# Kernel tuning notes

Measured on AMD Instinct MI355X. Metric: run time of the kernel, lower is better.

## Reference

```python
import jax, jax.numpy as jnp
import numpy as np


def setup_inputs() -> dict:
    key = jax.random.key(0)
    k1, k2 = jax.random.split(key)
    B, S, H, D = 4, 2048, 12, 64
    v = jax.random.normal(k1, (B, S, H, D), dtype=jnp.float32)
    # learned per-head positional weights, sorted ascending along last dim
    # (mirrors torch.sort(torch.randn(H, S), dim=-1)[0])
    w = jnp.sort(jax.random.normal(k2, (H, S), dtype=jnp.float32), axis=-1)
    return {"v": v, "w": w}


def reference(v, w):
    # PositionalBias._naive
    # v: [B, S, H, D]; w: [H, S_max]
    B, S, H, D = v.shape
    seq_len = S - 2  # v[:, 1:-1] is the non-special-token span
    w_ = w[:, :seq_len]  # [H, seq_len]
    # _construct_bias builds bias[h, l, j] = w[h, |l - j|] (symmetric Toeplitz)
    pos = jnp.arange(seq_len)
    idx = jnp.abs(pos[:, None] - pos[None, :])  # [seq_len, seq_len]
    bias = w_[:, idx]  # [H, seq_len, seq_len]
    # zero-pad one row/col on each side -> [H, S, S]
    bias = jnp.pad(bias, ((0, 0), (1, 1), (1, 1)))
    # z_pb: [1, S, H]
    z_pb = jnp.sum(bias, axis=-1).T[None, :, :]
    # pbv: [B, S, H, D]
    pbv = jnp.einsum('nlhd,hlj->njhd', v, bias)
    return (pbv, z_pb)
```

## Files before the change

kernel.cpp:

```cpp
#include <hip/hip_runtime.h>
#include <hip/hip_bf16.h>


typedef short short8 __attribute__((ext_vector_type(8)));
typedef float floatx4 __attribute__((ext_vector_type(4)));

typedef const __attribute__((address_space(1))) void gvoid_t;
typedef __attribute__((address_space(3))) void lvoid_t;

__device__ __forceinline__ unsigned short f2bf(float f) {
  union { __hip_bfloat16 b; unsigned short u; } cv;
  cv.b = __float2bfloat16(f);
  return cv.u;
}

__global__ __launch_bounds__(256) void transpose_kernel(const float* __restrict__ v,
                                                        unsigned short* __restrict__ vb) {
  __shared__ float tile[64][65];
  const int lt = blockIdx.x;
  const int h  = blockIdx.y;
  const int n  = blockIdx.z;
  const int tid = threadIdx.x;
  const int l0 = lt * 64;
  {
    const int d  = tid & 63;
    const int r0 = tid >> 6;
    #pragma unroll
    for (int rr = 0; rr < 16; ++rr) {
      int ll = r0 * 16 + rr;
      tile[ll][d] = v[(((size_t)n * 2048 + (l0 + ll)) * 12 + h) * 64 + d];
    }
  }
  __syncthreads();
  {
    const int d = tid >> 2;
    const int q = tid & 3;
    unsigned short buf[16] __attribute__((aligned(16)));
    #pragma unroll
    for (int jj = 0; jj < 16; ++jj) {
      int l = l0 + q * 16 + jj;
      float f = tile[q * 16 + jj][d];
      buf[jj] = (l == 0 || l == 2047) ? (unsigned short)0 : f2bf(f);
    }
    unsigned short* dst = vb + ((size_t)h * 256 + n * 64 + d) * 2048 + l0 + q * 16;
    *(uint4*)dst       = *(const uint4*)&buf[0];
    *(uint4*)(dst + 8) = *(const uint4*)&buf[8];
  }
}

__global__ __launch_bounds__(256) void zpb_kernel(const float* __restrict__ w,
                                                  float* __restrict__ zout) {
  __shared__ float wv[2048];
  __shared__ float pfx[2048];
  __shared__ float wsum[4];
  const int h = blockIdx.x;
  const int tid = threadIdx.x;
  const float* wh = w + (size_t)h * 2048;
  for (int i = tid; i < 2048; i += 256) wv[i] = (i < 2046) ? wh[i] : 0.f;
  __syncthreads();
  const int base = tid * 8;
  float run0 = 0.f;
  #pragma unroll
  for (int k = 0; k < 8; ++k) run0 += wv[base + k];
  float x = run0;
  #pragma unroll
  for (int d = 1; d < 64; d <<= 1) {
    float y = __shfl_up(x, d);
    if ((tid & 63) >= d) x += y;
  }
  if ((tid & 63) == 63) wsum[tid >> 6] = x;
  __syncthreads();
  const int wid = tid >> 6;
  float woff = 0.f;
  #pragma unroll
  for (int u = 0; u < 3; ++u) { float t = wsum[u]; if (u < wid) woff += t; }
  float excl = x + woff - run0;
  float pr = excl;
  #pragma unroll
  for (int k = 0; k < 8; ++k) { pr += wv[base + k]; pfx[base + k] = pr; }
  __syncthreads();
  for (int i = tid; i < 2046; i += 256) {
    float z = pfx[i] + pfx[2045 - i] - wv[0];
    zout[(size_t)(i + 1) * 12 + h] = z;
  }
  if (tid == 0) { zout[h] = 0.f; zout[(size_t)2047 * 12 + h] = 0.f; }
}

__global__ __launch_bounds__(256, 2) void gemm_kernel(const float* __restrict__ w,
                                                      const unsigned short* __restrict__ vb,
                                                      float* __restrict__ out) {
  __shared__ __attribute__((aligned(16))) short Tls[8 * 2184];
  __shared__ __attribute__((aligned(16))) short vt[2][128][32];

  const int jt  = blockIdx.x;
  const int ndt = blockIdx.y;
  const int h   = blockIdx.z;
  const int tid = threadIdx.x;
  const int lane = tid & 63;
  const int wid  = tid >> 6;
  const int wm = wid >> 1, wn = wid & 1;
  const int lm = lane & 15, quad = lane >> 4;
  const int jb = jt * 128;

  const float* wh = w + (size_t)h * 2048;
  for (int g = tid; g < 8 * 273; g += 256) {
    int c  = g / 273;
    int p8 = (g - c * 273) * 8;
    unsigned short buf[8] __attribute__((aligned(16)));
    #pragma unroll
    for (int i = 0; i < 8; ++i) {
      int t = 127 + jb - (p8 + i) - c;
      int a = t < 0 ? -t : t;
      buf[i] = (a <= 2045) ? f2bf(wh[a]) : (unsigned short)0;
    }
    *(short8*)&Tls[c * 2184 + p8] = *(const short8*)buf;
  }
  __syncthreads();

  const int nd0 = ndt * 128;
  const int jw  = jb + wm * 64;
  const int ndw = nd0 + wn * 64;
  const unsigned short* vbp = vb + (size_t)h * 256 * 2048;

  floatx4 acc[4][4];
  #pragma unroll
  for (int ma = 0; ma < 4; ++ma)
    #pragma unroll
    for (int na = 0; na < 4; ++na)
      acc[ma][na] = (floatx4){0.f, 0.f, 0.f, 0.f};

  const int pbase = 127 + quad * 8 - wm * 64 - lm;
  auto load_af = [&](int g16, int l0) -> short8 {
    int p0 = l0 + g16 + pbase;
    int c  = p0 & 7;
    return *(const short8*)&Tls[c * 2184 + (p0 - c)];
  };

  short8 a4 = load_af(-48, 0);
  short8 a5 = load_af(-32, 0);

  #pragma unroll 1
  for (int l0 = 0; l0 < 2048; l0 += 64) {
    #pragma unroll
    for (int s = 0; s < 2; ++s) {
      #pragma unroll
      for (int u = 0; u < 2; ++u) {
        int e  = wid * 2 + u;
        int r0 = e * 16;
        int grow = nd0 + r0 + (lane >> 2);
        int gcol = l0 + s * 32 + (lane & 3) * 8;
        const unsigned short* g = vbp + (size_t)grow * 2048 + gcol;
        __builtin_amdgcn_global_load_lds((gvoid_t*)g, (lvoid_t*)&vt[s][r0][0], 16, 0, 0);
      }
    }
    asm volatile("s_waitcnt vmcnt(0)" ::: "memory");
    __syncthreads();

    short8 afr[6];
    afr[0] = a4; afr[1] = a5;
    afr[2] = load_af(-16, l0);
    afr[3] = load_af(0,   l0);
    afr[4] = load_af(16,  l0);
    afr[5] = load_af(32,  l0);
    a4 = afr[4]; a5 = afr[5];

    #pragma unroll
    for (int kc = 0; kc < 2; ++kc) {
      short8 bfr[4];
      #pragma unroll
      for (int na = 0; na < 4; ++na)
        bfr[na] = *(const short8*)&vt[kc][wn * 64 + na * 16 + lm][quad * 8];
      #pragma unroll
      for (int ma = 0; ma < 4; ++ma) {
        short8 af = afr[(kc ? 5 : 3) - ma];
        #pragma unroll
        for (int na = 0; na < 4; ++na)
          acc[ma][na] = __builtin_amdgcn_mfma_f32_16x16x32_bf16(af, bfr[na], acc[ma][na], 0, 0, 0);
      }
    }
    __syncthreads();
  }

  #pragma unroll
  for (int ma = 0; ma < 4; ++ma) {
    #pragma unroll
    for (int na = 0; na < 4; ++na) {
      floatx4 c = acc[ma][na];
      int ndv = ndw + na * 16 + lm;
      int n = ndv >> 6, d = ndv & 63;
      #pragma unroll
      for (int r = 0; r < 4; ++r) {
        int j = jw + ma * 16 + quad * 4 + r;
        float val = (j == 0 || j == 2047) ? 0.f : c[r];
        out[(size_t)n * 1572864 + (size_t)j * 768 + h * 64 + d] = val;
      }
    }
  }
}

extern "C" void kernel_launch(void* const* d_in, const int* in_sizes, int n_in,
                              void* d_out, int out_size, void* d_ws, size_t ws_size,
                              hipStream_t stream) {
  const float* v = (const float*)d_in[0];
  const float* w = (const float*)d_in[1];
  float* out = (float*)d_out;
  unsigned short* vb = (unsigned short*)d_ws;

  transpose_kernel<<<dim3(32, 12, 4), 256, 0, stream>>>(v, vb);
  zpb_kernel<<<dim3(12), 256, 0, stream>>>(w, out + 6291456);
  gemm_kernel<<<dim3(16, 2, 12), 256, 0, stream>>>(w, vb, out);
}
```

Before: 126.5 us.

## Double-buffer GEMM V tiles, swizzle LDS layout, halve N tile, fuse prep kernels

Folds the z_pb prefix-sum kernel into the transpose kernel as an extra grid column, which saves one launch. The transposed V is now written with an XOR swizzle on 16-byte chunks so the GEMM's LDS fragment reads avoid bank conflicts. The GEMM N tile shrinks from 128 to 64, doubling the grid to 768 blocks with an occupancy hint of 3, and the V tile for the next step is prefetched into a second LDS buffer while the current one is computed. The cost is more redundant Toeplitz-table construction per block and half the register reuse of A fragments.

```diff
diff --git a/kernel.cpp b/kernel.cpp
--- a/kernel.cpp
+++ b/kernel.cpp
@@ -14,13 +14,53 @@
   return cv.u;
 }
 
-__global__ __launch_bounds__(256) void transpose_kernel(const float* __restrict__ v,
-                                                        unsigned short* __restrict__ vb) {
-  __shared__ float tile[64][65];
+__global__ __launch_bounds__(256) void prep_kernel(const float* __restrict__ v,
+                                                   const float* __restrict__ w,
+                                                   unsigned short* __restrict__ vb,
+                                                   float* __restrict__ zout) {
+  __shared__ float smem[64 * 65];
   const int lt = blockIdx.x;
   const int h  = blockIdx.y;
   const int n  = blockIdx.z;
   const int tid = threadIdx.x;
+
+  if (lt == 32) {
+    if (n != 0) return;
+    float* wv  = smem;
+    float* pfx = smem + 2048;
+    __shared__ float wsum[4];
+    const float* wh = w + (size_t)h * 2048;
+    for (int i = tid; i < 2048; i += 256) wv[i] = (i < 2046) ? wh[i] : 0.f;
+    __syncthreads();
+    const int base = tid * 8;
+    float run0 = 0.f;
+    #pragma unroll
+    for (int k = 0; k < 8; ++k) run0 += wv[base + k];
+    float x = run0;
+    #pragma unroll
+    for (int d = 1; d < 64; d <<= 1) {
+      float y = __shfl_up(x, d);
+      if ((tid & 63) >= d) x += y;
+    }
+    if ((tid & 63) == 63) wsum[tid >> 6] = x;
+    __syncthreads();
+    const int wid = tid >> 6;
+    float woff = 0.f;
+    #pragma unroll
+    for (int u = 0; u < 3; ++u) { float t = wsum[u]; if (u < wid) woff += t; }
+    float pr = x + woff - run0;
+    #pragma unroll
+    for (int k = 0; k < 8; ++k) { pr += wv[base + k]; pfx[base + k] = pr; }
+    __syncthreads();
+    for (int i = tid; i < 2046; i += 256) {
+      float z = pfx[i] + pfx[2045 - i] - wv[0];
+      zout[(size_t)(i + 1) * 12 + h] = z;
+    }
+    if (tid == 0) { zout[h] = 0.f; zout[(size_t)2047 * 12 + h] = 0.f; }
+    return;
+  }
+
+  float (*tile)[65] = (float(*)[65])smem;
   const int l0 = lt * 64;
   {
     const int d  = tid & 63;
@@ -35,6 +75,8 @@
   {
     const int d = tid >> 2;
     const int q = tid & 3;
+    const int nd = n * 64 + d;
+    const int sw = nd & 7;
     unsigned short buf[16] __attribute__((aligned(16)));
     #pragma unroll
     for (int jj = 0; jj < 16; ++jj) {
@@ -42,55 +84,18 @@
       float f = tile[q * 16 + jj][d];
       buf[jj] = (l == 0 || l == 2047) ? (unsigned short)0 : f2bf(f);
     }
-    unsigned short* dst = vb + ((size_t)h * 256 + n * 64 + d) * 2048 + l0 + q * 16;
-    *(uint4*)dst       = *(const uint4*)&buf[0];
-    *(uint4*)(dst + 8) = *(const uint4*)&buf[8];
-  }
-}
-
-__global__ __launch_bounds__(256) void zpb_kernel(const float* __restrict__ w,
-                                                  float* __restrict__ zout) {
-  __shared__ float wv[2048];
-  __shared__ float pfx[2048];
-  __shared__ float wsum[4];
-  const int h = blockIdx.x;
-  const int tid = threadIdx.x;
-  const float* wh = w + (size_t)h * 2048;
-  for (int i = tid; i < 2048; i += 256) wv[i] = (i < 2046) ? wh[i] : 0.f;
-  __syncthreads();
-  const int base = tid * 8;
-  float run0 = 0.f;
-  #pragma unroll
-  for (int k = 0; k < 8; ++k) run0 += wv[base + k];
-  float x = run0;
-  #pragma unroll
-  for (int d = 1; d < 64; d <<= 1) {
-    float y = __shfl_up(x, d);
-    if ((tid & 63) >= d) x += y;
-  }
-  if ((tid & 63) == 63) wsum[tid >> 6] = x;
-  __syncthreads();
-  const int wid = tid >> 6;
-  float woff = 0.f;
-  #pragma unroll
-  for (int u = 0; u < 3; ++u) { float t = wsum[u]; if (u < wid) woff += t; }
-  float excl = x + woff - run0;
-  float pr = excl;
-  #pragma unroll
-  for (int k = 0; k < 8; ++k) { pr += wv[base + k]; pfx[base + k] = pr; }
-  __syncthreads();
-  for (int i = tid; i < 2046; i += 256) {
-    float z = pfx[i] + pfx[2045 - i] - wv[0];
-    zout[(size_t)(i + 1) * 12 + h] = z;
-  }
-  if (tid == 0) { zout[h] = 0.f; zout[(size_t)2047 * 12 + h] = 0.f; }
-}
-
-__global__ __launch_bounds__(256, 2) void gemm_kernel(const float* __restrict__ w,
+    unsigned short* dstrow = vb + ((size_t)h * 256 + nd) * 2048 + l0;
+    int c0 = (2 * q) ^ sw, c1 = (2 * q + 1) ^ sw;
+    *(uint4*)(dstrow + c0 * 8) = *(const uint4*)&buf[0];
+    *(uint4*)(dstrow + c1 * 8) = *(const uint4*)&buf[8];
+  }
+}
+
+__global__ __launch_bounds__(256, 3) void gemm_kernel(const float* __restrict__ w,
                                                       const unsigned short* __restrict__ vb,
                                                       float* __restrict__ out) {
   __shared__ __attribute__((aligned(16))) short Tls[8 * 2184];
-  __shared__ __attribute__((aligned(16))) short vt[2][128][32];
+  __shared__ __attribute__((aligned(16))) short vt[2][64][64];
 
   const int jt  = blockIdx.x;
   const int ndt = blockIdx.y;
@@ -101,6 +106,19 @@
   const int wm = wid >> 1, wn = wid & 1;
   const int lm = lane & 15, quad = lane >> 4;
   const int jb = jt * 128;
+  const int nd0 = ndt * 64;
+  const unsigned short* vbp = vb + (size_t)h * 256 * 2048;
+
+  auto issue_dma = [&](int l0, int b) {
+    #pragma unroll
+    for (int u = 0; u < 2; ++u) {
+      int e = wid * 2 + u;
+      const unsigned short* g = vbp + (size_t)(nd0 + e * 8 + (lane >> 3)) * 2048 + l0 + (lane & 7) * 8;
+      __builtin_amdgcn_global_load_lds((gvoid_t*)g, (lvoid_t*)&vt[b][e * 8][0], 16, 0, 0);
+    }
+  };
+
+  issue_dma(0, 0);
 
   const float* wh = w + (size_t)h * 2048;
   for (int g = tid; g < 8 * 273; g += 256) {
@@ -117,16 +135,11 @@
   }
   __syncthreads();
 
-  const int nd0 = ndt * 128;
-  const int jw  = jb + wm * 64;
-  const int ndw = nd0 + wn * 64;
-  const unsigned short* vbp = vb + (size_t)h * 256 * 2048;
-
-  floatx4 acc[4][4];
+  floatx4 acc[4][2];
   #pragma unroll
   for (int ma = 0; ma < 4; ++ma)
     #pragma unroll
-    for (int na = 0; na < 4; ++na)
+    for (int na = 0; na < 2; ++na)
       acc[ma][na] = (floatx4){0.f, 0.f, 0.f, 0.f};
 
   const int pbase = 127 + quad * 8 - wm * 64 - lm;
@@ -139,23 +152,10 @@
   short8 a4 = load_af(-48, 0);
   short8 a5 = load_af(-32, 0);
 
-  #pragma unroll 1
-  for (int l0 = 0; l0 < 2048; l0 += 64) {
-    #pragma unroll
-    for (int s = 0; s < 2; ++s) {
-      #pragma unroll
-      for (int u = 0; u < 2; ++u) {
-        int e  = wid * 2 + u;
-        int r0 = e * 16;
-        int grow = nd0 + r0 + (lane >> 2);
-        int gcol = l0 + s * 32 + (lane & 3) * 8;
-        const unsigned short* g = vbp + (size_t)grow * 2048 + gcol;
-        __builtin_amdgcn_global_load_lds((gvoid_t*)g, (lvoid_t*)&vt[s][r0][0], 16, 0, 0);
-      }
-    }
-    asm volatile("s_waitcnt vmcnt(0)" ::: "memory");
-    __syncthreads();
-
+  #pragma unroll 2
+  for (int t = 0; t < 32; ++t) {
+    const int l0 = t * 64;
+    const int b  = t & 1;
     short8 afr[6];
     afr[0] = a4; afr[1] = a5;
     afr[2] = load_af(-16, l0);
@@ -164,27 +164,35 @@
     afr[5] = load_af(32,  l0);
     a4 = afr[4]; a5 = afr[5];
 
+    asm volatile("s_waitcnt vmcnt(0)" ::: "memory");
+    __syncthreads();
+    if (t < 31) issue_dma(l0 + 64, b ^ 1);
+
     #pragma unroll
     for (int kc = 0; kc < 2; ++kc) {
-      short8 bfr[4];
+      short8 bfr[2];
       #pragma unroll
-      for (int na = 0; na < 4; ++na)
-        bfr[na] = *(const short8*)&vt[kc][wn * 64 + na * 16 + lm][quad * 8];
+      for (int na = 0; na < 2; ++na) {
+        int row  = wn * 32 + na * 16 + lm;
+        int slot = (kc * 4 + quad) ^ (lm & 7);
+        bfr[na] = *(const short8*)&vt[b][row][slot * 8];
+      }
       #pragma unroll
       for (int ma = 0; ma < 4; ++ma) {
         short8 af = afr[(kc ? 5 : 3) - ma];
         #pragma unroll
-        for (int na = 0; na < 4; ++na)
+        for (int na = 0; na < 2; ++na)
           acc[ma][na] = __builtin_amdgcn_mfma_f32_16x16x32_bf16(af, bfr[na], acc[ma][na], 0, 0, 0);
       }
     }
-    __syncthreads();
-  }
-
+  }
+
+  const int jw  = jb + wm * 64;
+  const int ndw = nd0 + wn * 32;
   #pragma unroll
   for (int ma = 0; ma < 4; ++ma) {
     #pragma unroll
-    for (int na = 0; na < 4; ++na) {
+    for (int na = 0; na < 2; ++na) {
       floatx4 c = acc[ma][na];
       int ndv = ndw + na * 16 + lm;
       int n = ndv >> 6, d = ndv & 63;
@@ -206,7 +214,6 @@
   float* out = (float*)d_out;
   unsigned short* vb = (unsigned short*)d_ws;
 
-  transpose_kernel<<<dim3(32, 12, 4), 256, 0, stream>>>(v, vb);
-  zpb_kernel<<<dim3(12), 256, 0, stream>>>(w, out + 6291456);
-  gemm_kernel<<<dim3(16, 2, 12), 256, 0, stream>>>(w, vb, out);
-}
+  prep_kernel<<<dim3(33, 12, 4), 256, 0, stream>>>(v, w, vb, out + 6291456);
+  gemm_kernel<<<dim3(16, 4, 12), 256, 0, stream>>>(w, vb, out);
+}
```

Result: faster. 123.7 us (-2.2%).
